# Performance work log

Measured on AMD Instinct MI355X. Metric: run time of the kernel, lower is better.

## Reference

```python
import jax, jax.numpy as jnp
import numpy as np

N_DOF = 7
HIDDEN = 256
BATCH = 32768
L_DIAG_OFFSET = 1e-3
FRICTION_EPS = 100.0


def setup_inputs() -> dict:
    key = jax.random.key(0)
    ks = jax.random.split(key, 16)
    n, H, B = N_DOF, HIDDEN, BATCH
    ntril = n * (n - 1) // 2

    def xavier(k, shape):
        fan_out, fan_in = shape
        std = (2.0 / (fan_in + fan_out)) ** 0.5
        return jax.random.normal(k, shape, jnp.float32) * std

    return {
        "q":   jax.random.normal(ks[0], (B, n), jnp.float32),
        "qd":  jax.random.normal(ks[1], (B, n), jnp.float32),
        "qdd": jax.random.normal(ks[2], (B, n), jnp.float32),
        # MLP trunk (hidden_depth = 3)
        "W0": xavier(ks[3], (H, n)),  "b0": jnp.zeros((H,), jnp.float32),
        "W1": xavier(ks[4], (H, H)),  "b1": jnp.zeros((H,), jnp.float32),
        "W2": xavier(ks[5], (H, H)),  "b2": jnp.zeros((H,), jnp.float32),
        # heads: gravity g, Cholesky diagonal, Cholesky strict-lower
        "Wg":  xavier(ks[6], (n, H)),     "bg":  jnp.zeros((n,), jnp.float32),
        "Wld": xavier(ks[7], (n, H)),     "bld": jnp.zeros((n,), jnp.float32),
        "Wlt": xavier(ks[8], (ntril, H)), "blt": jnp.zeros((ntril,), jnp.float32),
        # friction model parameters (init 0.1 each)
        "fd": jnp.full((n,), 0.1, jnp.float32),
        "fc": jnp.full((n,), 0.1, jnp.float32),
        "fs": jnp.full((n,), 0.1, jnp.float32),
        "fv": jnp.full((n,), 0.1, jnp.float32),
    }


def reference(q, qd, qdd, W0, b0, W1, b1, W2, b2, Wg, bg, Wld, bld, Wlt, blt,
              fd, fc, fs, fv):
    n = N_DOF
    B = q.shape[0]
    sp = jax.nn.softplus

    def net(qq):  # qq: [n] single sample
        h = sp(W0 @ qq + b0)
        h = sp(W1 @ h + b1)
        h = sp(W2 @ h + b2)
        g = Wg @ h + bg                      # [n]
        Ld_raw = Wld @ h + bld               # [n]
        Ld = sp(Ld_raw)                      # softplus diag activation
        Lt = Wlt @ h + blt                   # [n_tril]
        return (Ld, Lt), (g, Ld, Lt, Ld_raw)

    # per-sample Jacobians of (L_diag, L_tril) wrt q (forward mode, n_dof tangents)
    (jLd, jLt), (g, Ld, Lt, Ld_raw) = jax.vmap(jax.jacfwd(net, has_aux=True))(q)
    # jLd: [B,n,n], jLt: [B,ntril,n]

    idx = np.arange(n)
    rows, cols = np.tril_indices(n, -1)

    L = (jnp.zeros((B, n, n), q.dtype)
         .at[:, idx, idx].set(Ld)
         .at[:, rows, cols].set(Lt)
         + L_DIAG_OFFSET * jnp.eye(n, dtype=q.dtype))          # [B,n,n]
    L_dq = (jnp.zeros((B, n, n, n), q.dtype)
            .at[:, idx, idx, :].set(jLd)
            .at[:, rows, cols, :].set(jLt))                    # [B,n,n,n] (last = dq)

    LT = jnp.swapaxes(L, 1, 2)
    L_dqT = jnp.swapaxes(L_dq, 1, 2)

    Hm = jnp.einsum('bij,bjk->bik', L, LT)                      # mass matrix
    L_dt = jnp.einsum('bijc,bc->bij', L_dq, qd)                 # dL/dt
    L_dtT = jnp.swapaxes(L_dt, 1, 2)
    H_dt = jnp.einsum('bij,bjk->bik', L, L_dtT) + jnp.einsum('bij,bjk->bik', L_dt, LT)
    H_dq = (jnp.einsum('bijc,bjk->bikc', L_dq, LT)
            + jnp.einsum('bij,bjkc->bikc', L, L_dqT))           # [B,n,n,n]
    H_dq_qd = jnp.einsum('bijc,bj->bic', H_dq, qd)
    qdT_H_dq_qd = jnp.einsum('bi,bic->bc', qd, H_dq_qd)
    c = jnp.einsum('bij,bj->bi', H_dt, qd) - 0.5 * qdT_H_dq_qd  # Coriolis

    fv_c = jnp.clip(fv, 1e-3, None)
    tau_fric = (fc + fs * jnp.exp(-qd ** 2 / fv_c)) * jnp.tanh(FRICTION_EPS * qd) + fd * qd

    tau_pred = jnp.einsum('bij,bj->bi', Hm, qdd) + c + g + tau_fric
    return (tau_pred, Hm, c, g, tau_fric, Ld_raw)
```

## Files before the change

### kernel.cpp

```cpp
#include <hip/hip_runtime.h>
#include <cmath>

#define NDOF 7
#define HID  256
#define SPW  8
#define NCOL 64

typedef __bf16 bf16x8 __attribute__((ext_vector_type(8)));
typedef float  f32x4  __attribute__((ext_vector_type(4)));

__device__ __forceinline__ float softplus_fast(float x){
    float e = __expf(-fabsf(x));
    return fmaxf(x, 0.0f) + __logf(1.0f + e);
}
__device__ __forceinline__ float sigmoid_fast(float x){
    float e  = __expf(-fabsf(x));
    float rc = 1.0f / (1.0f + e);
    return (x >= 0.0f) ? rc : e * rc;
}
__device__ __forceinline__ float tanh_fast(float y){
    float e2 = __expf(-2.0f * fabsf(y));
    float t  = (1.0f - e2) / (1.0f + e2);
    return (y >= 0.0f) ? t : -t;
}

__global__ void convert_weights(const float* __restrict__ W1, const float* __restrict__ W2,
                                const float* __restrict__ Wg, const float* __restrict__ Wld,
                                const float* __restrict__ Wlt, __bf16* __restrict__ ws)
{
    int i = blockIdx.x * 256 + threadIdx.x;
    if (i < 65536)        ws[i] = (__bf16)W1[i];
    else if (i < 131072)  ws[i] = (__bf16)W2[i - 65536];
    else if (i < 143360) {
        int j = i - 131072;
        int r = j >> 8, k = j & 255;
        float v = 0.0f;
        if (r < 7)       v = Wg [r * HID + k];
        else if (r < 14) v = Wld[(r - 7) * HID + k];
        else if (r < 35) v = Wlt[(r - 14) * HID + k];
        ws[i] = (__bf16)v;
    }
}

__launch_bounds__(256, 2)
__global__ void dln_main(
    const float* __restrict__ q,  const float* __restrict__ qd, const float* __restrict__ qdd,
    const float* __restrict__ W0, const float* __restrict__ b0,
    const float* __restrict__ b1, const float* __restrict__ b2,
    const float* __restrict__ bg, const float* __restrict__ bld, const float* __restrict__ blt,
    const float* __restrict__ fd, const float* __restrict__ fc,
    const float* __restrict__ fs, const float* __restrict__ fv,
    const __bf16* __restrict__ wsb,
    float* __restrict__ out, int Btot)
{
    __shared__ __bf16 Xs[NCOL * HID];
    __shared__ float  SCR[35 * 64];
    __shared__ float  qs[SPW][NDOF], qds[SPW][NDOF], qdds[SPW][NDOF];
    __shared__ float  Ls[SPW][7][7], vsh[SPW][7][7], ldts[SPW][7][7];
    __shared__ float  ubuf[SPW][8], wbuf[SPW][8], sgld[SPW][8], ldraw_s[SPW][8];

    const int tid = threadIdx.x;
    const int w   = tid >> 6;
    const int l   = tid & 63;
    const int lo  = l & 15;
    const int hi  = l >> 4;
    const int s0g = blockIdx.x * SPW;

    if (tid < SPW * NDOF){
        int s = tid / NDOF, d = tid % NDOF;
        qs[s][d]   = q  [(s0g + s) * NDOF + d];
        qds[s][d]  = qd [(s0g + s) * NDOF + d];
        qdds[s][d] = qdd[(s0g + s) * NDOF + d];
    }

    int  srcl[4]; bool isprim[4];
    #pragma unroll
    for (int ni = 0; ni < 4; ++ni){
        int col   = ni * 16 + lo;
        int s     = (col < 8) ? col : (col - 8) / 7;
        srcl[ni]  = (l & ~15) | s;
        isprim[ni]= (col < 8);
    }
    __syncthreads();

    {
        float w0r[NDOF];
        #pragma unroll
        for (int d = 0; d < NDOF; ++d) w0r[d] = W0[tid * NDOF + d];
        float b0v = b0[tid];
        #pragma unroll
        for (int s = 0; s < SPW; ++s){
            float z = b0v;
            #pragma unroll
            for (int d = 0; d < NDOF; ++d) z = fmaf(w0r[d], qs[s][d], z);
            float h = softplus_fast(z), sg = sigmoid_fast(z);
            Xs[s * HID + (tid ^ ((s & 7) << 3))] = (__bf16)h;
            #pragma unroll
            for (int d = 0; d < NDOF; ++d){
                int col = 8 + s * 7 + d;
                Xs[col * HID + (tid ^ ((col & 7) << 3))] = (__bf16)(sg * w0r[d]);
            }
        }
    }
    __syncthreads();

    auto hidden_layer = [&](const __bf16* __restrict__ Wb, const float* __restrict__ bp){
        f32x4 acc[4][4];
        #pragma unroll
        for (int mi = 0; mi < 4; ++mi)
            #pragma unroll
            for (int ni = 0; ni < 4; ++ni) acc[mi][ni] = (f32x4){0.f,0.f,0.f,0.f};

        #pragma unroll 2
        for (int kk = 0; kk < 8; ++kk){
            const int k0 = kk * 32 + hi * 8;
            bf16x8 a[4], bfr[4];
            #pragma unroll
            for (int mi = 0; mi < 4; ++mi)
                a[mi] = *reinterpret_cast<const bf16x8*>(Wb + (w * 64 + mi * 16 + lo) * HID + k0);
            #pragma unroll
            for (int ni = 0; ni < 4; ++ni){
                int col = ni * 16 + lo;
                bfr[ni] = *reinterpret_cast<const bf16x8*>(Xs + col * HID + (k0 ^ ((col & 7) << 3)));
            }
            #pragma unroll
            for (int mi = 0; mi < 4; ++mi)
                #pragma unroll
                for (int ni = 0; ni < 4; ++ni)
                    acc[mi][ni] = __builtin_amdgcn_mfma_f32_16x16x32_bf16(a[mi], bfr[ni], acc[mi][ni], 0, 0, 0);
        }
        __syncthreads();

        #pragma unroll
        for (int mi = 0; mi < 4; ++mi){
            const int row0 = w * 64 + mi * 16 + hi * 4;
            float4 b4 = *reinterpret_cast<const float4*>(bp + row0);
            float h[4], sg[4];
            #pragma unroll
            for (int r = 0; r < 4; ++r){
                float z  = acc[mi][0][r] + ((const float*)&b4)[r];
                float e  = __expf(-fabsf(z));
                float rc = 1.0f / (1.0f + e);
                h[r]  = fmaxf(z, 0.0f) + __logf(1.0f + e);
                sg[r] = (z >= 0.0f) ? rc : e * rc;
            }
            #pragma unroll
            for (int ni = 0; ni < 4; ++ni){
                int col = ni * 16 + lo;
                union { uint2 u2; __bf16 b[4]; } pk;
                #pragma unroll
                for (int r = 0; r < 4; ++r){
                    float sgb = __shfl(sg[r], srcl[ni]);
                    float v   = isprim[ni] ? h[r] : sgb * acc[mi][ni][r];
                    pk.b[r] = (__bf16)v;
                }
                *reinterpret_cast<uint2*>(Xs + col * HID + (row0 ^ ((col & 7) << 3))) = pk.u2;
            }
        }
        __syncthreads();
    };

    hidden_layer(wsb,           b1);
    hidden_layer(wsb + 65536,   b2);

    {
        const __bf16* Wh = wsb + 131072;
        if (w < 3){
            f32x4 hacc[4];
            #pragma unroll
            for (int ni = 0; ni < 4; ++ni) hacc[ni] = (f32x4){0.f,0.f,0.f,0.f};
            #pragma unroll 2
            for (int kk = 0; kk < 8; ++kk){
                const int k0 = kk * 32 + hi * 8;
                bf16x8 a = *reinterpret_cast<const bf16x8*>(Wh + (w * 16 + lo) * HID + k0);
                #pragma unroll
                for (int ni = 0; ni < 4; ++ni){
                    int col = ni * 16 + lo;
                    bf16x8 bfr = *reinterpret_cast<const bf16x8*>(Xs + col * HID + (k0 ^ ((col & 7) << 3)));
                    hacc[ni] = __builtin_amdgcn_mfma_f32_16x16x32_bf16(a, bfr, hacc[ni], 0, 0, 0);
                }
            }
            #pragma unroll
            for (int ni = 0; ni < 4; ++ni)
                #pragma unroll
                for (int r = 0; r < 4; ++r){
                    int row = w * 16 + hi * 4 + r;
                    if (row < 35) SCR[row * 64 + ni * 16 + lo] = hacc[ni][r];
                }
        }
    }
    __syncthreads();

    {
        const int s = tid >> 5;
        const int t = tid & 31;

        if (t < 7){
            int i = t;
            float lr = SCR[(7 + i) * 64 + s] + bld[i];
            ldraw_s[s][i] = lr;
            sgld[s][i]    = sigmoid_fast(lr);
            for (int j = 0; j < 7; ++j){
                float val;
                if (j == i)      val = softplus_fast(lr) + 1e-3f;
                else if (j < i)  val = SCR[(14 + (i*(i-1))/2 + j) * 64 + s] + blt[(i*(i-1))/2 + j];
                else             val = 0.f;
                Ls[s][i][j] = val;
            }
        }
        __syncthreads();

        auto LDQ = [&](int i, int j, int c)->float{
            if (i == j) return sgld[s][i] * SCR[(7 + i) * 64 + 8 + s * 7 + c];
            if (i >  j) return SCR[(14 + (i*(i-1))/2 + j) * 64 + 8 + s * 7 + c];
            return 0.f;
        };

        if (t < 7){
            float u = 0.f;
            for (int j = 0; j < 7; ++j) u = fmaf(qds[s][j], Ls[s][j][t], u);
            ubuf[s][t] = u;
            for (int m = 0; m < 7; ++m){
                float v = 0.f;
                for (int j = 0; j < 7; ++j) v = fmaf(qds[s][j], LDQ(j, m, t), v);
                vsh[s][m][t] = v;
            }
            for (int k = 0; k < 7; ++k){
                float a = 0.f;
                for (int c2 = 0; c2 < 7; ++c2) a = fmaf(LDQ(t, k, c2), qds[s][c2], a);
                ldts[s][t][k] = a;
            }
        }
        __syncthreads();

        if (t < 7){
            float w2 = 0.f;
            for (int c2 = 0; c2 < 7; ++c2) w2 = fmaf(vsh[s][t][c2], qds[s][c2], w2);
            wbuf[s][t] = w2;
        }
        __syncthreads();

        if (t < 7){
            const int i  = t;
            const int Sg = s0g + s;
            float c1 = 0.f;
            for (int k = 0; k < 7; ++k)
                c1 += Ls[s][i][k] * wbuf[s][k] + ldts[s][i][k] * ubuf[s][k];
            float qh = 0.f;
            for (int m = 0; m < 7; ++m) qh = fmaf(ubuf[s][m], vsh[s][m][i], qh);
            float cfin = c1 - qh;
            float hm[7];
            for (int j = 0; j < 7; ++j){
                float a = 0.f;
                for (int k = 0; k < 7; ++k) a = fmaf(Ls[s][i][k], Ls[s][j][k], a);
                hm[j] = a;
            }
            float gv  = SCR[i * 64 + s] + bg[i];
            float qdv = qds[s][i];
            float fvc = fmaxf(fv[i], 1e-3f);
            float tf  = (fc[i] + fs[i] * __expf(-qdv * qdv / fvc)) * tanh_fast(100.0f * qdv) + fd[i] * qdv;
            float tp  = cfin + gv + tf;
            for (int j = 0; j < 7; ++j) tp = fmaf(hm[j], qdds[s][j], tp);

            const int B = Btot;
            out[Sg * 7 + i] = tp;
            float* o1 = out + (size_t)B * 7;
            for (int j = 0; j < 7; ++j) o1[(size_t)Sg * 49 + i * 7 + j] = hm[j];
            out[(size_t)B * 56 + Sg * 7 + i] = cfin;
            out[(size_t)B * 63 + Sg * 7 + i] = gv;
            out[(size_t)B * 70 + Sg * 7 + i] = tf;
            out[(size_t)B * 77 + Sg * 7 + i] = ldraw_s[s][i];
        }
    }
}

extern "C" void kernel_launch(void* const* d_in, const int* in_sizes, int n_in,
                              void* d_out, int out_size, void* d_ws, size_t ws_size,
                              hipStream_t stream) {
    const float* q   = (const float*)d_in[0];
    const float* qd  = (const float*)d_in[1];
    const float* qdd = (const float*)d_in[2];
    const float* W0  = (const float*)d_in[3];
    const float* b0  = (const float*)d_in[4];
    const float* W1  = (const float*)d_in[5];
    const float* b1  = (const float*)d_in[6];
    const float* W2  = (const float*)d_in[7];
    const float* b2  = (const float*)d_in[8];
    const float* Wg  = (const float*)d_in[9];
    const float* bg  = (const float*)d_in[10];
    const float* Wld = (const float*)d_in[11];
    const float* bld = (const float*)d_in[12];
    const float* Wlt = (const float*)d_in[13];
    const float* blt = (const float*)d_in[14];
    const float* fd  = (const float*)d_in[15];
    const float* fc  = (const float*)d_in[16];
    const float* fs  = (const float*)d_in[17];
    const float* fv  = (const float*)d_in[18];

    const int Btot = in_sizes[0] / NDOF;
    __bf16* wsb = (__bf16*)d_ws;

    convert_weights<<<dim3(560), dim3(256), 0, stream>>>(W1, W2, Wg, Wld, Wlt, wsb);
    dln_main<<<dim3(Btot / SPW), dim3(256), 0, stream>>>(q, qd, qdd, W0, b0,
                                                         b1, b2, bg, bld, blt,
                                                         fd, fc, fs, fv,
                                                         wsb, (float*)d_out, Btot);
}
```

Measured before the change: 283.5 us.

## Run first MLP layer as MFMA, alias LDS buffers, raise occupancy to four blocks

The scalar first layer becomes an MFMA GEMM over a zero-padded bf16 copy of W0, with [q; one-hot tangent] columns staged in shared memory. The sigmoid broadcast now goes through a small shared buffer instead of wave shuffles. The scratch buffers for the head and the Lagrangian stage reuse the activation tile's shared memory, and launch bounds ask for four blocks per CU. Together these aim to shrink LDS and register pressure so more blocks run concurrently, at the cost of extra zero-fill, an added layer pass, and possible register spills.

New measurement: 267.4 us. 5.7% less time.

```diff
diff --git a/kernel.cpp b/kernel.cpp
--- a/kernel.cpp
+++ b/kernel.cpp
@@ -9,6 +9,11 @@
 typedef __bf16 bf16x8 __attribute__((ext_vector_type(8)));
 typedef float  f32x4  __attribute__((ext_vector_type(4)));
 
+#define OFF_W2 65536
+#define OFF_WH 131072
+#define OFF_W0 143360
+#define WS_TOT 151552
+
 __device__ __forceinline__ float softplus_fast(float x){
     float e = __expf(-fabsf(x));
     return fmaxf(x, 0.0f) + __logf(1.0f + e);
@@ -26,38 +31,112 @@
 
 __global__ void convert_weights(const float* __restrict__ W1, const float* __restrict__ W2,
                                 const float* __restrict__ Wg, const float* __restrict__ Wld,
-                                const float* __restrict__ Wlt, __bf16* __restrict__ ws)
+                                const float* __restrict__ Wlt, const float* __restrict__ W0,
+                                __bf16* __restrict__ ws)
 {
     int i = blockIdx.x * 256 + threadIdx.x;
-    if (i < 65536)        ws[i] = (__bf16)W1[i];
-    else if (i < 131072)  ws[i] = (__bf16)W2[i - 65536];
-    else if (i < 143360) {
-        int j = i - 131072;
+    if (i < OFF_W2)        ws[i] = (__bf16)W1[i];
+    else if (i < OFF_WH)   ws[i] = (__bf16)W2[i - OFF_W2];
+    else if (i < OFF_W0) {
+        int j = i - OFF_WH;
         int r = j >> 8, k = j & 255;
         float v = 0.0f;
         if (r < 7)       v = Wg [r * HID + k];
         else if (r < 14) v = Wld[(r - 7) * HID + k];
         else if (r < 35) v = Wlt[(r - 14) * HID + k];
         ws[i] = (__bf16)v;
-    }
-}
-
-__launch_bounds__(256, 2)
+    } else if (i < WS_TOT) {
+        int j = i - OFF_W0;
+        int r = j >> 5, k = j & 31;
+        ws[i] = (__bf16)((k < 7) ? W0[r * 7 + k] : 0.0f);
+    }
+}
+
+template<int KK>
+__device__ __forceinline__ void mlp_layer(
+    const __bf16* __restrict__ Wb, int astride, const float* __restrict__ bp,
+    __bf16* Xs, __bf16 (*sgbuf)[264],
+    int w, int lo, int hi, const int* scol, bool prim)
+{
+    f32x4 acc[4][4];
+    #pragma unroll
+    for (int mi = 0; mi < 4; ++mi)
+        #pragma unroll
+        for (int ni = 0; ni < 4; ++ni) acc[mi][ni] = (f32x4){0.f,0.f,0.f,0.f};
+
+    #pragma unroll 2
+    for (int kk = 0; kk < KK; ++kk){
+        const int k0 = kk * 32 + hi * 8;
+        bf16x8 a[4], bfr[4];
+        #pragma unroll
+        for (int mi = 0; mi < 4; ++mi)
+            a[mi] = *reinterpret_cast<const bf16x8*>(Wb + (w * 64 + mi * 16 + lo) * astride + k0);
+        #pragma unroll
+        for (int ni = 0; ni < 4; ++ni){
+            int col = ni * 16 + lo;
+            bfr[ni] = *reinterpret_cast<const bf16x8*>(Xs + col * HID + (k0 ^ ((col & 7) << 3)));
+        }
+        #pragma unroll
+        for (int mi = 0; mi < 4; ++mi)
+            #pragma unroll
+            for (int ni = 0; ni < 4; ++ni)
+                acc[mi][ni] = __builtin_amdgcn_mfma_f32_16x16x32_bf16(a[mi], bfr[ni], acc[mi][ni], 0, 0, 0);
+    }
+    __syncthreads();
+
+    float h[4][4];
+    #pragma unroll
+    for (int mi = 0; mi < 4; ++mi){
+        const int row0 = w * 64 + mi * 16 + hi * 4;
+        float4 b4 = *reinterpret_cast<const float4*>(bp + row0);
+        union { uint2 u2; __bf16 b[4]; } sp;
+        #pragma unroll
+        for (int r = 0; r < 4; ++r){
+            float z  = acc[mi][0][r] + ((const float*)&b4)[r];
+            float e  = __expf(-fabsf(z));
+            float rc = 1.0f / (1.0f + e);
+            h[mi][r] = fmaxf(z, 0.0f) + __logf(1.0f + e);
+            sp.b[r]  = (__bf16)((z >= 0.0f) ? rc : e * rc);
+        }
+        if (lo < 8) *reinterpret_cast<uint2*>(&sgbuf[lo][row0]) = sp.u2;
+    }
+    asm volatile("s_waitcnt lgkmcnt(0)" ::: "memory");
+
+    #pragma unroll
+    for (int mi = 0; mi < 4; ++mi){
+        const int row0 = w * 64 + mi * 16 + hi * 4;
+        #pragma unroll
+        for (int ni = 0; ni < 4; ++ni){
+            union { uint2 u2; __bf16 b[4]; } sg;
+            sg.u2 = *reinterpret_cast<const uint2*>(&sgbuf[scol[ni]][row0]);
+            int col = ni * 16 + lo;
+            union { uint2 u2; __bf16 b[4]; } pk;
+            #pragma unroll
+            for (int r = 0; r < 4; ++r){
+                float v = (ni == 0 && prim) ? h[mi][r] : (float)sg.b[r] * acc[mi][ni][r];
+                pk.b[r] = (__bf16)v;
+            }
+            *reinterpret_cast<uint2*>(Xs + col * HID + (row0 ^ ((col & 7) << 3))) = pk.u2;
+        }
+    }
+    __syncthreads();
+}
+
+__launch_bounds__(256, 4)
 __global__ void dln_main(
     const float* __restrict__ q,  const float* __restrict__ qd, const float* __restrict__ qdd,
-    const float* __restrict__ W0, const float* __restrict__ b0,
-    const float* __restrict__ b1, const float* __restrict__ b2,
+    const float* __restrict__ b0, const float* __restrict__ b1, const float* __restrict__ b2,
     const float* __restrict__ bg, const float* __restrict__ bld, const float* __restrict__ blt,
     const float* __restrict__ fd, const float* __restrict__ fc,
     const float* __restrict__ fs, const float* __restrict__ fv,
     const __bf16* __restrict__ wsb,
     float* __restrict__ out, int Btot)
 {
-    __shared__ __bf16 Xs[NCOL * HID];
-    __shared__ float  SCR[35 * 64];
-    __shared__ float  qs[SPW][NDOF], qds[SPW][NDOF], qdds[SPW][NDOF];
-    __shared__ float  Ls[SPW][7][7], vsh[SPW][7][7], ldts[SPW][7][7];
-    __shared__ float  ubuf[SPW][8], wbuf[SPW][8], sgld[SPW][8], ldraw_s[SPW][8];
+    __shared__ __align__(16) unsigned char LDSB[32768];
+    __shared__ __bf16 sgbuf[SPW][264];
+    __shared__ float  qs[SPW][NDOF], qds_[SPW][NDOF], qdds_[SPW][NDOF];
+
+    __bf16* Xs = (__bf16*)LDSB;
 
     const int tid = threadIdx.x;
     const int w   = tid >> 6;
@@ -65,129 +144,78 @@
     const int lo  = l & 15;
     const int hi  = l >> 4;
     const int s0g = blockIdx.x * SPW;
+    const bool prim = (lo < 8);
 
     if (tid < SPW * NDOF){
         int s = tid / NDOF, d = tid % NDOF;
-        qs[s][d]   = q  [(s0g + s) * NDOF + d];
-        qds[s][d]  = qd [(s0g + s) * NDOF + d];
-        qdds[s][d] = qdd[(s0g + s) * NDOF + d];
-    }
-
-    int  srcl[4]; bool isprim[4];
+        qs[s][d]    = q  [(s0g + s) * NDOF + d];
+        qds_[s][d]  = qd [(s0g + s) * NDOF + d];
+        qdds_[s][d] = qdd[(s0g + s) * NDOF + d];
+    }
+
+    int scol[4];
     #pragma unroll
     for (int ni = 0; ni < 4; ++ni){
-        int col   = ni * 16 + lo;
-        int s     = (col < 8) ? col : (col - 8) / 7;
-        srcl[ni]  = (l & ~15) | s;
-        isprim[ni]= (col < 8);
-    }
-    __syncthreads();
+        int col  = ni * 16 + lo;
+        scol[ni] = (col < 8) ? col : (col - 8) / 7;
+    }
 
     {
-        float w0r[NDOF];
-        #pragma unroll
-        for (int d = 0; d < NDOF; ++d) w0r[d] = W0[tid * NDOF + d];
-        float b0v = b0[tid];
-        #pragma unroll
-        for (int s = 0; s < SPW; ++s){
-            float z = b0v;
-            #pragma unroll
-            for (int d = 0; d < NDOF; ++d) z = fmaf(w0r[d], qs[s][d], z);
-            float h = softplus_fast(z), sg = sigmoid_fast(z);
-            Xs[s * HID + (tid ^ ((s & 7) << 3))] = (__bf16)h;
-            #pragma unroll
-            for (int d = 0; d < NDOF; ++d){
-                int col = 8 + s * 7 + d;
-                Xs[col * HID + (tid ^ ((col & 7) << 3))] = (__bf16)(sg * w0r[d]);
-            }
-        }
-    }
-    __syncthreads();
-
-    auto hidden_layer = [&](const __bf16* __restrict__ Wb, const float* __restrict__ bp){
-        f32x4 acc[4][4];
-        #pragma unroll
-        for (int mi = 0; mi < 4; ++mi)
-            #pragma unroll
-            for (int ni = 0; ni < 4; ++ni) acc[mi][ni] = (f32x4){0.f,0.f,0.f,0.f};
-
+        int col = tid >> 2, part = tid & 3;
+        uint4 z4 = {0,0,0,0};
+        *reinterpret_cast<uint4*>(Xs + col * HID + part * 16)     = z4;
+        *reinterpret_cast<uint4*>(Xs + col * HID + part * 16 + 8) = z4;
+    }
+    __syncthreads();
+    if (tid < 56){
+        int s = tid / 7, d = tid % 7;
+        Xs[s * HID + (d ^ ((s & 7) << 3))] = (__bf16)qs[s][d];
+        int c = 8 + s * 7 + d;
+        Xs[c * HID + (d ^ ((c & 7) << 3))] = (__bf16)1.0f;
+    }
+    __syncthreads();
+
+    mlp_layer<1>(wsb + OFF_W0, 32,  b0, Xs, sgbuf, w, lo, hi, scol, prim);
+    mlp_layer<8>(wsb,          HID, b1, Xs, sgbuf, w, lo, hi, scol, prim);
+    mlp_layer<8>(wsb + OFF_W2, HID, b2, Xs, sgbuf, w, lo, hi, scol, prim);
+
+    f32x4 hacc[4];
+    #pragma unroll
+    for (int ni = 0; ni < 4; ++ni) hacc[ni] = (f32x4){0.f,0.f,0.f,0.f};
+    if (w < 3){
+        const __bf16* Wh = wsb + OFF_WH;
         #pragma unroll 2
         for (int kk = 0; kk < 8; ++kk){
             const int k0 = kk * 32 + hi * 8;
-            bf16x8 a[4], bfr[4];
-            #pragma unroll
-            for (int mi = 0; mi < 4; ++mi)
-                a[mi] = *reinterpret_cast<const bf16x8*>(Wb + (w * 64 + mi * 16 + lo) * HID + k0);
+            bf16x8 a = *reinterpret_cast<const bf16x8*>(Wh + (w * 16 + lo) * HID + k0);
             #pragma unroll
             for (int ni = 0; ni < 4; ++ni){
                 int col = ni * 16 + lo;
-                bfr[ni] = *reinterpret_cast<const bf16x8*>(Xs + col * HID + (k0 ^ ((col & 7) << 3)));
-            }
-            #pragma unroll
-            for (int mi = 0; mi < 4; ++mi)
-                #pragma unroll
-                for (int ni = 0; ni < 4; ++ni)
-                    acc[mi][ni] = __builtin_amdgcn_mfma_f32_16x16x32_bf16(a[mi], bfr[ni], acc[mi][ni], 0, 0, 0);
-        }
-        __syncthreads();
-
-        #pragma unroll
-        for (int mi = 0; mi < 4; ++mi){
-            const int row0 = w * 64 + mi * 16 + hi * 4;
-            float4 b4 = *reinterpret_cast<const float4*>(bp + row0);
-            float h[4], sg[4];
+                bf16x8 bfr = *reinterpret_cast<const bf16x8*>(Xs + col * HID + (k0 ^ ((col & 7) << 3)));
+                hacc[ni] = __builtin_amdgcn_mfma_f32_16x16x32_bf16(a, bfr, hacc[ni], 0, 0, 0);
+            }
+        }
+    }
+    __syncthreads();
+
+    float* SCR = (float*)LDSB;
+    float* TB  = (float*)LDSB + 2304;
+    #define LSA(s,i,j) TB[(s)*49+(i)*7+(j)]
+    #define VSH(s,i,j) TB[392+(s)*49+(i)*7+(j)]
+    #define LDT(s,i,j) TB[784+(s)*49+(i)*7+(j)]
+    #define UB(s,k)    TB[1176+(s)*8+(k)]
+    #define WB2(s,k)   TB[1240+(s)*8+(k)]
+    #define SGL(s,k)   TB[1304+(s)*8+(k)]
+    #define LDR(s,k)   TB[1368+(s)*8+(k)]
+
+    if (w < 3){
+        #pragma unroll
+        for (int ni = 0; ni < 4; ++ni)
             #pragma unroll
             for (int r = 0; r < 4; ++r){
-                float z  = acc[mi][0][r] + ((const float*)&b4)[r];
-                float e  = __expf(-fabsf(z));
-                float rc = 1.0f / (1.0f + e);
-                h[r]  = fmaxf(z, 0.0f) + __logf(1.0f + e);
-                sg[r] = (z >= 0.0f) ? rc : e * rc;
-            }
-            #pragma unroll
-            for (int ni = 0; ni < 4; ++ni){
-                int col = ni * 16 + lo;
-                union { uint2 u2; __bf16 b[4]; } pk;
-                #pragma unroll
-                for (int r = 0; r < 4; ++r){
-                    float sgb = __shfl(sg[r], srcl[ni]);
-                    float v   = isprim[ni] ? h[r] : sgb * acc[mi][ni][r];
-                    pk.b[r] = (__bf16)v;
-                }
-                *reinterpret_cast<uint2*>(Xs + col * HID + (row0 ^ ((col & 7) << 3))) = pk.u2;
-            }
-        }
-        __syncthreads();
-    };
-
-    hidden_layer(wsb,           b1);
-    hidden_layer(wsb + 65536,   b2);
-
-    {
-        const __bf16* Wh = wsb + 131072;
-        if (w < 3){
-            f32x4 hacc[4];
-            #pragma unroll
-            for (int ni = 0; ni < 4; ++ni) hacc[ni] = (f32x4){0.f,0.f,0.f,0.f};
-            #pragma unroll 2
-            for (int kk = 0; kk < 8; ++kk){
-                const int k0 = kk * 32 + hi * 8;
-                bf16x8 a = *reinterpret_cast<const bf16x8*>(Wh + (w * 16 + lo) * HID + k0);
-                #pragma unroll
-                for (int ni = 0; ni < 4; ++ni){
-                    int col = ni * 16 + lo;
-                    bf16x8 bfr = *reinterpret_cast<const bf16x8*>(Xs + col * HID + (k0 ^ ((col & 7) << 3)));
-                    hacc[ni] = __builtin_amdgcn_mfma_f32_16x16x32_bf16(a, bfr, hacc[ni], 0, 0, 0);
-                }
-            }
-            #pragma unroll
-            for (int ni = 0; ni < 4; ++ni)
-                #pragma unroll
-                for (int r = 0; r < 4; ++r){
-                    int row = w * 16 + hi * 4 + r;
-                    if (row < 35) SCR[row * 64 + ni * 16 + lo] = hacc[ni][r];
-                }
-        }
+                int row = w * 16 + hi * 4 + r;
+                if (row < 35) SCR[row * 64 + ni * 16 + lo] = hacc[ni][r];
+            }
     }
     __syncthreads();
 
@@ -198,45 +226,45 @@
         if (t < 7){
             int i = t;
             float lr = SCR[(7 + i) * 64 + s] + bld[i];
-            ldraw_s[s][i] = lr;
-            sgld[s][i]    = sigmoid_fast(lr);
+            LDR(s, i) = lr;
+            SGL(s, i) = sigmoid_fast(lr);
             for (int j = 0; j < 7; ++j){
                 float val;
                 if (j == i)      val = softplus_fast(lr) + 1e-3f;
                 else if (j < i)  val = SCR[(14 + (i*(i-1))/2 + j) * 64 + s] + blt[(i*(i-1))/2 + j];
                 else             val = 0.f;
-                Ls[s][i][j] = val;
+                LSA(s, i, j) = val;
             }
         }
         __syncthreads();
 
         auto LDQ = [&](int i, int j, int c)->float{
-            if (i == j) return sgld[s][i] * SCR[(7 + i) * 64 + 8 + s * 7 + c];
+            if (i == j) return SGL(s, i) * SCR[(7 + i) * 64 + 8 + s * 7 + c];
             if (i >  j) return SCR[(14 + (i*(i-1))/2 + j) * 64 + 8 + s * 7 + c];
             return 0.f;
         };
 
         if (t < 7){
             float u = 0.f;
-            for (int j = 0; j < 7; ++j) u = fmaf(qds[s][j], Ls[s][j][t], u);
-            ubuf[s][t] = u;
+            for (int j = 0; j < 7; ++j) u = fmaf(qds_[s][j], LSA(s, j, t), u);
+            UB(s, t) = u;
             for (int m = 0; m < 7; ++m){
                 float v = 0.f;
-                for (int j = 0; j < 7; ++j) v = fmaf(qds[s][j], LDQ(j, m, t), v);
-                vsh[s][m][t] = v;
+                for (int j = 0; j < 7; ++j) v = fmaf(qds_[s][j], LDQ(j, m, t), v);
+                VSH(s, m, t) = v;
             }
             for (int k = 0; k < 7; ++k){
                 float a = 0.f;
-                for (int c2 = 0; c2 < 7; ++c2) a = fmaf(LDQ(t, k, c2), qds[s][c2], a);
-                ldts[s][t][k] = a;
+                for (int c2 = 0; c2 < 7; ++c2) a = fmaf(LDQ(t, k, c2), qds_[s][c2], a);
+                LDT(s, t, k) = a;
             }
         }
         __syncthreads();
 
         if (t < 7){
             float w2 = 0.f;
-            for (int c2 = 0; c2 < 7; ++c2) w2 = fmaf(vsh[s][t][c2], qds[s][c2], w2);
-            wbuf[s][t] = w2;
+            for (int c2 = 0; c2 < 7; ++c2) w2 = fmaf(VSH(s, t, c2), qds_[s][c2], w2);
+            WB2(s, t) = w2;
         }
         __syncthreads();
 
@@ -245,22 +273,22 @@
             const int Sg = s0g + s;
             float c1 = 0.f;
             for (int k = 0; k < 7; ++k)
-                c1 += Ls[s][i][k] * wbuf[s][k] + ldts[s][i][k] * ubuf[s][k];
+                c1 += LSA(s, i, k) * WB2(s, k) + LDT(s, i, k) * UB(s, k);
             float qh = 0.f;
-            for (int m = 0; m < 7; ++m) qh = fmaf(ubuf[s][m], vsh[s][m][i], qh);
+            for (int m = 0; m < 7; ++m) qh = fmaf(UB(s, m), VSH(s, m, i), qh);
             float cfin = c1 - qh;
             float hm[7];
             for (int j = 0; j < 7; ++j){
                 float a = 0.f;
-                for (int k = 0; k < 7; ++k) a = fmaf(Ls[s][i][k], Ls[s][j][k], a);
+                for (int k = 0; k < 7; ++k) a = fmaf(LSA(s, i, k), LSA(s, j, k), a);
                 hm[j] = a;
             }
             float gv  = SCR[i * 64 + s] + bg[i];
-            float qdv = qds[s][i];
+            float qdv = qds_[s][i];
             float fvc = fmaxf(fv[i], 1e-3f);
             float tf  = (fc[i] + fs[i] * __expf(-qdv * qdv / fvc)) * tanh_fast(100.0f * qdv) + fd[i] * qdv;
             float tp  = cfin + gv + tf;
-            for (int j = 0; j < 7; ++j) tp = fmaf(hm[j], qdds[s][j], tp);
+            for (int j = 0; j < 7; ++j) tp = fmaf(hm[j], qdds_[s][j], tp);
 
             const int B = Btot;
             out[Sg * 7 + i] = tp;
@@ -269,7 +297,7 @@
             out[(size_t)B * 56 + Sg * 7 + i] = cfin;
             out[(size_t)B * 63 + Sg * 7 + i] = gv;
             out[(size_t)B * 70 + Sg * 7 + i] = tf;
-            out[(size_t)B * 77 + Sg * 7 + i] = ldraw_s[s][i];
+            out[(size_t)B * 77 + Sg * 7 + i] = LDR(s, i);
         }
     }
 }
@@ -300,9 +328,9 @@
     const int Btot = in_sizes[0] / NDOF;
     __bf16* wsb = (__bf16*)d_ws;
 
-    convert_weights<<<dim3(560), dim3(256), 0, stream>>>(W1, W2, Wg, Wld, Wlt, wsb);
-    dln_main<<<dim3(Btot / SPW), dim3(256), 0, stream>>>(q, qd, qdd, W0, b0,
-                                                         b1, b2, bg, bld, blt,
+    convert_weights<<<dim3(WS_TOT / 256), dim3(256), 0, stream>>>(W1, W2, Wg, Wld, Wlt, W0, wsb);
+    dln_main<<<dim3(Btot / SPW), dim3(256), 0, stream>>>(q, qd, qdd, b0, b1, b2,
+                                                         bg, bld, blt,
                                                          fd, fc, fs, fv,
                                                          wsb, (float*)d_out, Btot);
 }
```
